# Kernel optimization log

Hardware: AMD Instinct MI355X
Metric: run time of the kernel (lower is better)

The kernel has to match this reference:

```python
import jax, jax.numpy as jnp
import numpy as np
import math

HIDDEN = 768
HEADS = 12
HEAD_DIM = HIDDEN // HEADS
BLOCK = 256
TOPK = 3
BATCH = 2
SEQ = 2048


def setup_inputs() -> dict:
    key = jax.random.key(0)
    ks = jax.random.split(key, 5)
    s = 1.0 / math.sqrt(HIDDEN)
    return {
        "hidden_states": jax.random.normal(ks[0], (BATCH, SEQ, HIDDEN), jnp.float32),
        "Wq": jax.random.normal(ks[1], (HIDDEN, HIDDEN), jnp.float32) * s,
        "Wk": jax.random.normal(ks[2], (HIDDEN, HIDDEN), jnp.float32) * s,
        "Wv": jax.random.normal(ks[3], (HIDDEN, HIDDEN), jnp.float32) * s,
        "Wo": jax.random.normal(ks[4], (HIDDEN, HIDDEN), jnp.float32) * s,
    }


def _rope(x, sin, cos):
    # x: [B, H, S, D]; rotate-half RoPE
    d2 = x.shape[-1] // 2
    x1, x2 = x[..., :d2], x[..., d2:]
    return x * cos + jnp.concatenate([-x2, x1], axis=-1) * sin


def reference(hidden_states, Wq, Wk, Wv, Wo):
    B, S, Hd = hidden_states.shape
    H, D, bs, K = HEADS, HEAD_DIM, BLOCK, TOPK
    nb = S // bs  # number of key blocks
    scale = 1.0 / math.sqrt(D)

    def split_heads(x):
        return x.reshape(B, S, H, D).transpose(0, 2, 1, 3)  # [B,H,S,D]

    q = split_heads(hidden_states @ Wq.T)
    k = split_heads(hidden_states @ Wk.T)
    v = split_heads(hidden_states @ Wv.T)

    # rotary embedding (standard rotate-half RoPE, base 10000)
    inv_freq = 1.0 / (10000.0 ** (jnp.arange(0, D, 2, dtype=jnp.float32) / D))
    ang = jnp.arange(S, dtype=jnp.float32)[:, None] * inv_freq[None, :]  # [S, D/2]
    emb = jnp.concatenate([ang, ang], axis=-1)  # [S, D]
    sin, cos = jnp.sin(emb), jnp.cos(emb)
    q = _rope(q, sin, cos)
    k = _rope(k, sin, cos)

    # mean-pooled block representations of keys: [B,H,nb,D]
    block_reps = k.reshape(B, H, nb, bs, D).mean(axis=3)

    # routing scores: per-token score against each block rep
    bscores = jnp.einsum('bhsd,bhnd->bhsn', q, block_reps) * scale  # [B,H,S,nb]
    pos = jnp.arange(S)
    cur = pos // bs                       # current block of each query, [S]
    blk = jnp.arange(nb)
    future = blk[None, None, None, :] > cur[None, None, :, None]
    bscores = jnp.where(future, -jnp.inf, bscores)
    # current block is force-selected (score set to dtype max)
    is_cur = blk[None, None, None, :] == cur[None, None, :, None]
    bscores = jnp.where(is_cur, jnp.finfo(bscores.dtype).max, bscores)

    _, topk_idx = jax.lax.top_k(bscores, min(K, nb))  # [B,H,S,K]
    selected = jnp.sum(jax.nn.one_hot(topk_idx, nb, dtype=jnp.float32), axis=-2) > 0  # [B,H,S,nb]

    # per-key-position mask: key t allowed iff its block is selected for query i,
    # and within the current block only t <= i (matches original truncation).
    sel_t = selected[:, :, :, cur]                          # [B,H,Sq,Sk]
    intra_ok = (cur[None, :] != cur[:, None]) | (pos[None, :] <= pos[:, None])  # [Sq,Sk]
    mask = sel_t & intra_ok[None, None]

    scores = jnp.einsum('bhqd,bhkd->bhqk', q, k) * scale
    scores = jnp.where(mask, scores, -jnp.inf)
    probs = jax.nn.softmax(scores, axis=-1)
    out = jnp.einsum('bhqk,bhkd->bhqd', probs, v)

    out = out.transpose(0, 2, 1, 3).reshape(B, S, Hd)
    return out @ Wo.T
```

## Files before the change

### kernel.cpp

```cpp
#include <hip/hip_runtime.h>
#include <math.h>


#define HID   768
#define NH    12
#define DH    64
#define SEQN  2048
#define BATCH 2
#define NTOK  (BATCH*SEQN)
#define NB    8
#define BLKSZ 256
#define NEG_INF (-__builtin_huge_valf())
#define POS_INF (__builtin_huge_valf())
#define LO_SCALE 2048.0f
#define LO_INV   (1.0f/2048.0f)
#define EXP2C    0.18033688f

#define SPLIT_ROWS 1024
#define NBH   (BATCH*NH)

typedef unsigned short u16;
typedef _Float16 v8hf __attribute__((ext_vector_type(8)));
typedef float    v4f  __attribute__((ext_vector_type(4)));

__device__ __forceinline__ u16 f2h(float x) {
    _Float16 h = (_Float16)x;
    return __builtin_bit_cast(u16, h);
}
__device__ __forceinline__ float h2f(u16 u) {
    return (float)__builtin_bit_cast(_Float16, u);
}
__device__ __forceinline__ v8hf ldhf8(const u16* p) {
    return *reinterpret_cast<const v8hf*>(p);
}
__device__ __forceinline__ void g2lds16(const u16* g, u16* l) {
    __builtin_amdgcn_global_load_lds(
        (const __attribute__((address_space(1))) void*)g,
        (__attribute__((address_space(3))) void*)l, 16, 0, 0);
}
#define MFMA16(a, b, c) __builtin_amdgcn_mfma_f32_16x16x32_f16(a, b, c, 0, 0, 0)

__device__ const int g_uord[48] = {
    46,47,44,45,15,
    42,43,40,41,14,
    38,39,36,37,13,
    34,35,32,33,12,
    30,31,28,29,11,
    26,27,24,25,10,
    22,23,20,21, 9,
    18,19,16,17, 8,
     7, 6, 5, 4, 3, 2, 1, 0
};

__global__ __launch_bounds__(256)
void preproc_k(const float* __restrict__ X,  const float* __restrict__ Wq,
               const float* __restrict__ Wk, const float* __restrict__ Wv,
               const float* __restrict__ Wo, float2* __restrict__ tab,
               u16* __restrict__ Xh, u16* __restrict__ Xl,
               u16* __restrict__ Wq2, u16* __restrict__ Wk2,
               u16* __restrict__ Wv2, u16* __restrict__ Wo2)
{
    const int NW = HID * HID;
    const int id = blockIdx.x;
    const int tid = threadIdx.x;
    if (id < 3072) {
        const int i = (id * 256 + tid) * 4;
        const float4 x4 = *(const float4*)&X[i];
        const float xf[4] = {x4.x, x4.y, x4.z, x4.w};
        ushort4 h4, l4;
        u16* hp = (u16*)&h4; u16* lp = (u16*)&l4;
        #pragma unroll
        for (int j = 0; j < 4; j++) {
            const u16 h = f2h(xf[j]);
            hp[j] = h;
            lp[j] = f2h((xf[j] - h2f(h)) * LO_SCALE);
        }
        *(ushort4*)&Xh[i] = h4;
        *(ushort4*)&Xl[i] = l4;
    } else if (id < 5376) {
        const int j4 = ((id - 3072) * 256 + tid) * 4;
        const int z = j4 / NW, i = j4 - z * NW;
        const float* src = (z == 0) ? Wq : (z == 1) ? Wk : (z == 2) ? Wv : Wo;
        u16* dst = (z == 0) ? Wq2 : (z == 1) ? Wk2 : (z == 2) ? Wv2 : Wo2;
        const float4 x4 = *(const float4*)&src[i];
        const float xf[4] = {x4.x, x4.y, x4.z, x4.w};
        ushort4 h4, l4;
        u16* hp = (u16*)&h4; u16* lp = (u16*)&l4;
        #pragma unroll
        for (int j = 0; j < 4; j++) {
            const u16 h = f2h(xf[j]);
            hp[j] = h;
            lp[j] = f2h((xf[j] - h2f(h)) * LO_SCALE);
        }
        *(ushort4*)&dst[i] = h4;
        *(ushort4*)&dst[i + NW] = l4;
    } else {
        const int i = (id - 5376) * 256 + tid;
        const int s = i >> 5, f = i & 31;
        const double y  = exp((double)f * (log(10000.0) / 32.0));
        const float yf = (float)y;
        const float invf = 1.0f / yf;
        const float ang  = (float)s * invf;
        tab[i] = make_float2((float)sin((double)ang), (float)cos((double)ang));
    }
}

__device__ __forceinline__
void qkv_mainloop(const u16* __restrict__ Ah, const u16* __restrict__ Al,
                  const u16* __restrict__ Bh, const u16* __restrict__ Bl,
                  int m0, int nb0, bool hasC0,
                  u16* As, u16* Bs, v4f acc01[2][4], v4f acc2[2][4])
{
    const int tid = threadIdx.x;
    const int w = tid >> 6, lane = tid & 63;
    const int col = lane & 15, quad = lane >> 4;
    const int AOFF = 128 * 64, BOFF = 64 * 64;

    int a_row[4], a_gl[4];
    #pragma unroll
    for (int r = 0; r < 4; r++) {
        const int g = r * 256 + tid;
        a_row[r] = g >> 3;
        a_gl[r]  = (g & 7) ^ (a_row[r] & 7);
    }
    int b_row[2], b_gl[2];
    #pragma unroll
    for (int r = 0; r < 2; r++) {
        const int g = r * 256 + tid;
        b_row[r] = g >> 3;
        b_gl[r]  = (g & 7) ^ (b_row[r] & 7);
    }

    for (int itc = 0; itc < HID / 64; itc++) {
        const int k0 = itc * 64;
        __syncthreads();
        #pragma unroll
        for (int r = 0; r < 4; r++)
            g2lds16(Ah + (size_t)(m0 + a_row[r]) * HID + k0 + a_gl[r] * 8,
                    &As[(r * 256 + w * 64) * 8]);
        if (hasC0) {
            #pragma unroll
            for (int r = 0; r < 4; r++)
                g2lds16(Al + (size_t)(m0 + a_row[r]) * HID + k0 + a_gl[r] * 8,
                        &As[AOFF + (r * 256 + w * 64) * 8]);
        }
        #pragma unroll
        for (int r = 0; r < 2; r++) {
            g2lds16(Bh + (size_t)(nb0 + b_row[r]) * HID + k0 + b_gl[r] * 8,
                    &Bs[(r * 256 + w * 64) * 8]);
            g2lds16(Bl + (size_t)(nb0 + b_row[r]) * HID + k0 + b_gl[r] * 8,
                    &Bs[BOFF + (r * 256 + w * 64) * 8]);
        }
        __syncthreads();
        #pragma unroll
        for (int ks = 0; ks < 2; ks++) {
            v8hf afh[2], afl[2], bfh[4], bfl[4];
            #pragma unroll
            for (int mt = 0; mt < 2; mt++) {
                const int row = w * 32 + mt * 16 + col;
                const int gph = (ks * 4 + quad) ^ (row & 7);
                afh[mt] = ldhf8(&As[row * 64 + gph * 8]);
                if (hasC0) afl[mt] = ldhf8(&As[AOFF + row * 64 + gph * 8]);
            }
            #pragma unroll
            for (int nt = 0; nt < 4; nt++) {
                const int row = nt * 16 + col;
                const int gph = (ks * 4 + quad) ^ (row & 7);
                bfh[nt] = ldhf8(&Bs[row * 64 + gph * 8]);
                bfl[nt] = ldhf8(&Bs[BOFF + row * 64 + gph * 8]);
            }
            #pragma unroll
            for (int mt = 0; mt < 2; mt++)
                #pragma unroll
                for (int nt = 0; nt < 4; nt++) {
                    if (hasC0)
                        acc01[mt][nt] = MFMA16(afl[mt], bfh[nt], acc01[mt][nt]);
                    acc01[mt][nt] = MFMA16(afh[mt], bfl[nt], acc01[mt][nt]);
                    acc2[mt][nt]  = MFMA16(afh[mt], bfh[nt], acc2[mt][nt]);
                }
        }
    }
    __syncthreads();
}

__global__ __launch_bounds__(256, 3)
void qkv_fused_gemm_k(const u16* __restrict__ Xh, const u16* __restrict__ Xl,
                      const u16* __restrict__ Wq2, const u16* __restrict__ Wk2,
                      const u16* __restrict__ Wv2, const float2* __restrict__ tab,
                      float* __restrict__ q32, u16* __restrict__ kh16,
                      u16* __restrict__ vth, float* __restrict__ partial)
{
    __shared__ u16 As[2 * 128 * 64];
    __shared__ u16 Bs[2 * 64 * 64];
    float (*psum)[64] = (float(*)[64])As;

    const int NW = HID * HID;
    const int id    = blockIdx.x;
    const int xcd   = id & 7, loc = id >> 3;
    const int mtile = xcd * 4 + (loc & 3);
    const int ntile = loc >> 2;
    const int m0  = mtile * 128;
    const int mat = ntile / 12;
    const int nb0 = (ntile - mat * 12) * 64;
    const u16* Bh = (mat == 0) ? Wq2 : (mat == 1) ? Wk2 : Wv2;

    v4f acc01[2][4] = {}, acc2[2][4] = {};
    qkv_mainloop(Xh, Xl, Bh, Bh + NW, m0, nb0, mat != 2, As, Bs, acc01, acc2);

    v4f acc[2][4];
    #pragma unroll
    for (int mt = 0; mt < 2; mt++)
        #pragma unroll
        for (int nt = 0; nt < 4; nt++)
            #pragma unroll
            for (int r = 0; r < 4; r++)
                acc[mt][nt][r] = acc01[mt][nt][r] * LO_INV + acc2[mt][nt][r];

    const int tid = threadIdx.x;
    const int w = tid >> 6, lane = tid & 63;
    const int col = lane & 15, quad = lane >> 4;
    const int b = m0 >> 11;
    const int h = nb0 >> 6;
    const size_t bh = (size_t)b * NH + h;

    if (mat == 2) {
        #pragma unroll
        for (int nt = 0; nt < 4; nt++) {
            const int d = nt * 16 + col;
            #pragma unroll
            for (int mt = 0; mt < 2; mt++) {
                const int m = m0 + w * 32 + mt * 16 + quad * 4;
                const int s = m & (SEQN - 1);
                ushort4 pk = make_ushort4(f2h(acc[mt][nt][0]), f2h(acc[mt][nt][1]),
                                          f2h(acc[mt][nt][2]), f2h(acc[mt][nt][3]));
                *(ushort4*)&vth[(bh * DH + d) * SEQN + s] = pk;
            }
        }
        return;
    }

    float vsum[4] = {0.f, 0.f, 0.f, 0.f};
    #pragma unroll
    for (int mt = 0; mt < 2; mt++) {
        #pragma unroll
        for (int nt = 0; nt < 4; nt++) {
            const int d = nt * 16 + col;
            #pragma unroll
            for (int r = 0; r < 4; r++) {
                const int m = m0 + w * 32 + mt * 16 + quad * 4 + r;
                const int s = m & (SEQN - 1);
                const float part = acc[mt][nt ^ 2][r];
                const float2 sc = tab[(s << 5) + (d & 31)];
                const float val = (d < 32) ? acc[mt][nt][r] * sc.y - part * sc.x
                                           : acc[mt][nt][r] * sc.y + part * sc.x;
                const size_t idx = (bh * SEQN + s) * DH + d;
                if (mat == 0) {
                    q32[idx] = val;
                } else {
                    kh16[idx] = f2h(val);
                    vsum[nt] += val;
                }
            }
        }
    }
    if (mat == 1) {
        #pragma unroll
        for (int nt = 0; nt < 4; nt++) {
            float v = vsum[nt];
            v += __shfl_xor(v, 16);
            v += __shfl_xor(v, 32);
            if (quad == 0) psum[w][nt * 16 + col] = v;
        }
        __syncthreads();
        if (tid < 64) {
            const float s4 = (psum[0][tid] + psum[1][tid])
                           + (psum[2][tid] + psum[3][tid]);
            const int nblk = (m0 & (SEQN - 1)) >> 8;
            const int half = (m0 >> 7) & 1;
            partial[((bh * NB + nblk) * 2 + half) * 64 + tid] = s4;
        }
    }
}

__global__ __launch_bounds__(256, 3)
void out_gemm_mfma_k(const u16* __restrict__ Ah, const u16* __restrict__ Wo2,
                     float* __restrict__ C)
{
    __shared__ u16 As[64 * 64];
    __shared__ u16 Bs[2 * 64 * 64];
    const int BOFF = 64 * 64;

    const int NW = HID * HID;
    const int id    = blockIdx.x;
    const int xcd   = id & 7, loc = id >> 3;
    const int mtile = xcd * 8 + (loc & 7);
    const int ntile = loc >> 3;
    const int m0 = mtile * 64, n0 = ntile * 64;
    const int tid = threadIdx.x;
    const int w = tid >> 6, lane = tid & 63;
    const int col = lane & 15, quad = lane >> 4;

    const int r0 = tid >> 3,         gl0 = (tid & 7) ^ (r0 & 7);
    const int r1 = (256 + tid) >> 3, gl1 = ((256 + tid) & 7) ^ (r1 & 7);

    const u16* Bhp = Wo2;
    const u16* Blp = Wo2 + NW;

    v4f accL[4] = {}, accH[4] = {};
    for (int itc = 0; itc < HID / 64; itc++) {
        const int k0 = itc * 64;
        __syncthreads();
        g2lds16(Ah  + (size_t)(m0 + r0) * HID + k0 + gl0 * 8, &As[(w * 64) * 8]);
        g2lds16(Ah  + (size_t)(m0 + r1) * HID + k0 + gl1 * 8, &As[(256 + w * 64) * 8]);
        g2lds16(Bhp + (size_t)(n0 + r0) * HID + k0 + gl0 * 8, &Bs[(w * 64) * 8]);
        g2lds16(Bhp + (size_t)(n0 + r1) * HID + k0 + gl1 * 8, &Bs[(256 + w * 64) * 8]);
        g2lds16(Blp + (size_t)(n0 + r0) * HID + k0 + gl0 * 8, &Bs[BOFF + (w * 64) * 8]);
        g2lds16(Blp + (size_t)(n0 + r1) * HID + k0 + gl1 * 8, &Bs[BOFF + (256 + w * 64) * 8]);
        __syncthreads();
        #pragma unroll
        for (int ks = 0; ks < 2; ks++) {
            const int arow = w * 16 + col;
            v8hf a = ldhf8(&As[arow * 64 + (((ks * 4 + quad) ^ (arow & 7))) * 8]);
            #pragma unroll
            for (int nt = 0; nt < 4; nt++) {
                const int row = nt * 16 + col;
                const int g = (ks * 4 + quad) ^ (row & 7);
                accH[nt] = MFMA16(a, ldhf8(&Bs[row * 64 + g * 8]), accH[nt]);
                accL[nt] = MFMA16(a, ldhf8(&Bs[BOFF + row * 64 + g * 8]), accL[nt]);
            }
        }
    }

    #pragma unroll
    for (int nt = 0; nt < 4; nt++)
        #pragma unroll
        for (int r = 0; r < 4; r++) {
            const int m = m0 + w * 16 + quad * 4 + r;
            C[(size_t)m * HID + n0 + nt * 16 + col] =
                accL[nt][r] * LO_INV + accH[nt][r];
        }
}

__global__ __launch_bounds__(256, 4)
void moba_attn_k(const float* __restrict__ q32, const u16* __restrict__ kh16,
                 const u16* __restrict__ vth, const float* __restrict__ partial,
                 u16* __restrict__ aoh, float* __restrict__ po,
                 float* __restrict__ ml)
{
    __shared__ u16 kbuf[2][64 * 64];
    __shared__ u16 vbuf[2][64 * 64];
    __shared__ u16 plds[4][16][64];
    unsigned* s_uni = (unsigned*)&vbuf[1][0];
    float (*rs)[DH] = (float(*)[DH])&kbuf[0][0];
    unsigned* msk   = (unsigned*)&kbuf[0][1024];

    const int id  = blockIdx.x;
    const int xcd = id & 7, loc = id >> 3;
    const int bh  = xcd * 3 + loc / 48;
    const int u   = g_uord[loc % 48];
    int qb, split, stride;
    if (u < 16) { qb = u;                 split = 0;          stride = 1; }
    else        { qb = 16 + ((u - 16) >> 1); split = (u - 16) & 1; stride = 2; }
    const int q0  = qb * 64;
    const int cur = q0 >> 8;
    const int tid = threadIdx.x;
    const int wave = tid >> 6, lane = tid & 63;
    const int col = lane & 15, quad = lane >> 4;
    const int qw0 = q0 + wave * 16;
    const int qpos = qw0 + col;
    const size_t bhS = (size_t)bh * SEQN;
    const size_t bhV = (size_t)bh * DH;

    if (tid == 0) *s_uni = 0;
    for (int idx = tid; idx < NB * DH; idx += 256) {
        const int n = idx >> 6, d = idx & 63;
        const float* pp = &partial[(size_t)((bh * NB + n) * 2) * 64 + d];
        const double s = (double)pp[0] + (double)pp[64];
        rs[n][d] = (float)(s * (1.0 / 256.0));
    }
    __syncthreads();

    if (tid < 64) {
        const float* qv = &q32[(bhS + q0 + tid) * DH];
        double sc[NB];
        #pragma unroll
        for (int n = 0; n < NB; n++) sc[n] = 0.0;
        for (int c = 0; c < 16; c++) {
            const float4 t = *(const float4*)&qv[c * 4];
            #pragma unroll
            for (int n = 0; n < NB; n++) {
                sc[n] += (double)t.x * (double)rs[n][c * 4 + 0];
                sc[n] += (double)t.y * (double)rs[n][c * 4 + 1];
                sc[n] += (double)t.z * (double)rs[n][c * 4 + 2];
                sc[n] += (double)t.w * (double)rs[n][c * 4 + 3];
            }
        }
        #pragma unroll
        for (int n = 0; n < NB; n++) sc[n] *= 0.125;
        for (int n = cur + 1; n < NB; n++) sc[n] = -1e300;
        sc[cur] = 1e300;
        unsigned m = 0;
        for (int p = 0; p < 3; p++) {
            int bi = -1; double bv = 0.0;
            for (int n = 0; n < NB; n++) {
                if ((m >> n) & 1) continue;
                if (bi < 0 || sc[n] > bv) { bi = n; bv = sc[n]; }
            }
            m |= 1u << bi;
        }
        msk[tid] = m;
    }
    __syncthreads();

    const unsigned mymask = msk[wave * 16 + col];
    unsigned uw = mymask;
    #pragma unroll
    for (int off = 1; off < 16; off <<= 1) uw |= __shfl_xor(uw, off);
    if (lane == 0) atomicOr(s_uni, uw);
    const unsigned wmask = __builtin_amdgcn_readfirstlane(uw);

    v8hf qh[2], ql[2];
    #pragma unroll
    for (int ks = 0; ks < 2; ks++) {
        const float* qp = &q32[(bhS + qw0 + col) * DH + ks * 32 + quad * 8];
        float4 f0 = *(const float4*)qp;
        float4 f1 = *(const float4*)(qp + 4);
        float qf[8] = {f0.x, f0.y, f0.z, f0.w, f1.x, f1.y, f1.z, f1.w};
        union { u16 u[8]; v8hf h; } uh, ul;
        #pragma unroll
        for (int j = 0; j < 8; j++) {
            u16 hb = f2h(qf[j]);
            uh.u[j] = hb;
            ul.u[j] = f2h((qf[j] - h2f(hb)) * LO_SCALE);
        }
        qh[ks] = uh.h; ql[ks] = ul.h;
    }
    __syncthreads();
    const unsigned uni = __builtin_amdgcn_readfirstlane(*s_uni);

    int n_nxt = __builtin_ctz(uni), c_nxt = 0;
    bool has_nxt = true;
    auto c2max = [&](int n) { return (n == cur) ? ((q0 + 63 - n * BLKSZ) >> 6) : 3; };
    auto advance1 = [&]() {
        if (c_nxt < c2max(n_nxt)) { c_nxt++; return; }
        for (int nn = n_nxt + 1; nn < NB; nn++)
            if ((uni >> nn) & 1) { n_nxt = nn; c_nxt = 0; return; }
        has_nxt = false;
    };
    for (int i = 0; i < split; i++) if (has_nxt) advance1();
    int n_cur = n_nxt, c_cur = c_nxt;
    const bool cur_valid = has_nxt;

    const size_t srow0 = (size_t)bh * SPLIT_ROWS + (q0 - SPLIT_ROWS);

    if (!cur_valid) {
        if (stride == 2) {
            if (quad == 0) {
                const size_t r = srow0 + wave * 16 + col;
                ml[(r * 2 + split) * 2 + 0] = NEG_INF;
                ml[(r * 2 + split) * 2 + 1] = 0.f;
            }
            #pragma unroll
            for (int nt = 0; nt < 4; nt++)
                #pragma unroll
                for (int r = 0; r < 4; r++) {
                    const size_t rq = srow0 + wave * 16 + quad * 4 + r;
                    po[(rq * 2 + split) * 64 + nt * 16 + col] = 0.f;
                }
        }
        return;
    }
    for (int i = 0; i < stride; i++) if (has_nxt) advance1();

    const int sg_row0 = tid >> 3;
    const int sg_gl0  = (tid & 7) ^ (sg_row0 & 7);
    const int sg_row1 = (256 + tid) >> 3;
    const int sg_gl1  = ((256 + tid) & 7) ^ (sg_row1 & 7);
    auto stage = [&](int n, int c2, int buf) {
        const int kb = n * BLKSZ + c2 * 64;
        u16* kd = (u16*)kbuf[buf];
        u16* vd = (u16*)vbuf[buf];
        const size_t ks0 = (bhS + kb + sg_row0) * DH + sg_gl0 * 8;
        const size_t ks1 = (bhS + kb + sg_row1) * DH + sg_gl1 * 8;
        const size_t vs0 = (bhV + sg_row0) * SEQN + kb + sg_gl0 * 8;
        const size_t vs1 = (bhV + sg_row1) * SEQN + kb + sg_gl1 * 8;
        g2lds16(kh16 + ks0, kd + (wave * 64) * 8);
        g2lds16(kh16 + ks1, kd + (256 + wave * 64) * 8);
        g2lds16(vth + vs0, vd + (wave * 64) * 8);
        g2lds16(vth + vs1, vd + (256 + wave * 64) * 8);
    };

    const v4f zero4 = {0.f, 0.f, 0.f, 0.f};
    v4f oacc[4] = {zero4, zero4, zero4, zero4};
    float m_i = NEG_INF, l_i = 0.f;
    const int psw = (col & 7) << 1;

    stage(n_cur, c_cur, 0);
    int t = 0;
    while (true) {
        __syncthreads();
        if (has_nxt) stage(n_nxt, c_nxt, (t + 1) & 1);

        const int n  = n_cur;
        const int kb = n * BLKSZ + c_cur * 64;
        const bool iscur = (n == cur);
        const float selinf = ((mymask >> n) & 1) ? 0.f : POS_INF;
        const bool need_mask = iscur && (kb + 63 > qw0);
        const u16* kd = (const u16*)kbuf[t & 1];
        const u16* vd = (const u16*)vbuf[t & 1];

        if ((wmask >> n) & 1) {
            v4f sf[4];
            __builtin_amdgcn_s_setprio(1);
            #pragma unroll
            for (int mt = 0; mt < 4; mt++) {
                const int row = mt * 16 + col;
                const int r7 = row & 7;
                v8hf kh0 = ldhf8(&kd[(row * 8 + (quad ^ r7)) * 8]);
                v8hf kh1 = ldhf8(&kd[(row * 8 + ((4 + quad) ^ r7)) * 8]);
                v4f c = zero4;
                c = MFMA16(kh0, ql[0], c);
                c = MFMA16(kh1, ql[1], c);
                #pragma unroll
                for (int r = 0; r < 4; r++) c[r] *= LO_INV;
                c = MFMA16(kh0, qh[0], c);
                c = MFMA16(kh1, qh[1], c);
                sf[mt] = c;
            }
            __builtin_amdgcn_s_setprio(0);

            if (need_mask) {
                #pragma unroll
                for (int mt = 0; mt < 4; mt++)
                    #pragma unroll
                    for (int r = 0; r < 4; r++) {
                        const int kidx = kb + mt * 16 + quad * 4 + r;
                        sf[mt][r] = (kidx <= qpos) ? sf[mt][r] : NEG_INF;
                    }
            }

            const float t0 = fmaxf(fmaxf(sf[0][0], sf[0][1]), fmaxf(sf[0][2], sf[0][3]));
            const float t1 = fmaxf(fmaxf(sf[1][0], sf[1][1]), fmaxf(sf[1][2], sf[1][3]));
            const float t2 = fmaxf(fmaxf(sf[2][0], sf[2][1]), fmaxf(sf[2][2], sf[2][3]));
            const float t3 = fmaxf(fmaxf(sf[3][0], sf[3][1]), fmaxf(sf[3][2], sf[3][3]));
            float rm = fmaxf(fmaxf(t0, t1), fmaxf(t2, t3));
            rm = fmaxf(rm, __shfl_xor(rm, 16));
            rm = fmaxf(rm, __shfl_xor(rm, 32));
            rm = rm - selinf;

            const bool fast = __all(rm <= m_i + 8.0f) != 0;
            float mnew = m_i, alpha = 1.f;
            if (!fast) {
                mnew  = fmaxf(m_i, rm);
                alpha = (m_i == NEG_INF) ? 0.f : exp2f((m_i - mnew) * EXP2C);
            }
            const float biasC = ((mnew == NEG_INF) ? 0.f : mnew * EXP2C) + selinf;

            float lmt[4];
            #pragma unroll
            for (int mt = 0; mt < 4; mt++) {
                ushort4 hv;
                float p0 = exp2f(fmaf(sf[mt][0], EXP2C, -biasC));
                float p1 = exp2f(fmaf(sf[mt][1], EXP2C, -biasC));
                float p2 = exp2f(fmaf(sf[mt][2], EXP2C, -biasC));
                float p3 = exp2f(fmaf(sf[mt][3], EXP2C, -biasC));
                hv.x = f2h(p0); hv.y = f2h(p1); hv.z = f2h(p2); hv.w = f2h(p3);
                lmt[mt] = (p0 + p1) + (p2 + p3);
                *(ushort4*)&plds[wave][col][((mt * 4 + quad) ^ psw) * 4] = hv;
            }
            float lsum = (lmt[0] + lmt[1]) + (lmt[2] + lmt[3]);
            lsum += __shfl_xor(lsum, 16);
            lsum += __shfl_xor(lsum, 32);

            if (fast) {
                l_i = l_i + lsum;
            } else {
                l_i = l_i * alpha + lsum;
                m_i = mnew;
                float ar[4];
                #pragma unroll
                for (int r = 0; r < 4; r++) ar[r] = __shfl(alpha, quad * 4 + r, 16);
                #pragma unroll
                for (int nt = 0; nt < 4; nt++)
                    #pragma unroll
                    for (int r = 0; r < 4; r++) oacc[nt][r] *= ar[r];
            }

            __threadfence_block();

            __builtin_amdgcn_s_setprio(1);
            #pragma unroll
            for (int ks2 = 0; ks2 < 2; ks2++) {
                v8hf ph = ldhf8(&plds[wave][col][((ks2 * 8 + quad * 2) ^ psw) * 4]);
                #pragma unroll
                for (int nt = 0; nt < 4; nt++) {
                    const int row = nt * 16 + col;
                    const int g = (ks2 * 4 + quad) ^ (row & 7);
                    v8hf vh = ldhf8(&vd[(row * 8 + g) * 8]);
                    oacc[nt] = MFMA16(ph, vh, oacc[nt]);
                }
            }
            __builtin_amdgcn_s_setprio(0);
        }

        if (!has_nxt) break;
        n_cur = n_nxt; c_cur = c_nxt;
        for (int i = 0; i < stride; i++) if (has_nxt) advance1();
        t++;
    }

    if (stride == 2) {
        if (quad == 0) {
            const size_t r = srow0 + wave * 16 + col;
            ml[(r * 2 + split) * 2 + 0] = m_i;
            ml[(r * 2 + split) * 2 + 1] = l_i;
        }
        #pragma unroll
        for (int nt = 0; nt < 4; nt++)
            #pragma unroll
            for (int r = 0; r < 4; r++) {
                const size_t rq = srow0 + wave * 16 + quad * 4 + r;
                po[(rq * 2 + split) * 64 + nt * 16 + col] = oacc[nt][r];
            }
        return;
    }

    const int b = bh / NH, h = bh % NH;
    const float invl = 1.f / l_i;
    float ir[4];
    #pragma unroll
    for (int r = 0; r < 4; r++) ir[r] = __shfl(invl, quad * 4 + r, 16);
    #pragma unroll
    for (int nt = 0; nt < 4; nt++)
        #pragma unroll
        for (int r = 0; r < 4; r++) {
            const int qi = qw0 + quad * 4 + r;
            const size_t idx = ((size_t)b * SEQN + qi) * HID + h * DH + nt * 16 + col;
            aoh[idx] = f2h(oacc[nt][r] * ir[r]);
        }
}

__global__ __launch_bounds__(256)
void attn_combine_k(const float* __restrict__ po, const float* __restrict__ ml,
                    u16* __restrict__ aoh)
{
    const int g = blockIdx.x * 256 + threadIdx.x;
    const int d = g & 63;
    const size_t row = (size_t)(g >> 6);
    const int bh = (int)(row >> 10);
    const int qlocal = (int)(row & 1023);
    const float m0 = ml[(row * 2 + 0) * 2 + 0], l0 = ml[(row * 2 + 0) * 2 + 1];
    const float m1 = ml[(row * 2 + 1) * 2 + 0], l1 = ml[(row * 2 + 1) * 2 + 1];
    const float m  = fmaxf(m0, m1);
    const float a0 = (m0 == NEG_INF) ? 0.f : exp2f((m0 - m) * EXP2C);
    const float a1 = (m1 == NEG_INF) ? 0.f : exp2f((m1 - m) * EXP2C);
    const float o  = po[(row * 2 + 0) * 64 + d] * a0
                   + po[(row * 2 + 1) * 64 + d] * a1;
    const float inv = 1.f / (l0 * a0 + l1 * a1);
    const int b = bh / NH, h = bh % NH;
    const int q = SPLIT_ROWS + qlocal;
    aoh[((size_t)b * SEQN + q) * HID + h * DH + d] = f2h(o * inv);
}

extern "C" void kernel_launch(void* const* d_in, const int* in_sizes, int n_in,
                              void* d_out, int out_size, void* d_ws, size_t ws_size,
                              hipStream_t stream)
{
    const float* X  = (const float*)d_in[0];
    const float* Wq = (const float*)d_in[1];
    const float* Wk = (const float*)d_in[2];
    const float* Wv = (const float*)d_in[3];
    const float* Wo = (const float*)d_in[4];
    float* out = (float*)d_out;

    char* p = (char*)d_ws;
    float* q32 = (float*)p;                p += (size_t)NTOK*HID*4;
    u16* kh16 = (u16*)p;                   p += (size_t)NTOK*HID*2;
    u16* vth  = (u16*)p;                   p += (size_t)NTOK*HID*2;
    u16* Xh   = (u16*)p;                   p += (size_t)NTOK*HID*2;
    u16* Xl   = (u16*)p;                   p += (size_t)NTOK*HID*2;
    u16* Wq2  = (u16*)p;                   p += (size_t)HID*HID*2*2;
    u16* Wk2  = (u16*)p;                   p += (size_t)HID*HID*2*2;
    u16* Wv2  = (u16*)p;                   p += (size_t)HID*HID*2*2;
    u16* Wo2  = (u16*)p;                   p += (size_t)HID*HID*2*2;
    float* partial = (float*)p;            p += (size_t)BATCH*NH*NB*2*64*4;
    float* reps    = (float*)p;            p += (size_t)BATCH*NH*NB*DH*4;
    unsigned* selm = (unsigned*)p;         p += (size_t)BATCH*NH*SEQN*4;
    float2* tab    = (float2*)p;           p += (size_t)SEQN*32*8;
    u16* aoh = Xh;
    (void)reps; (void)selm;

    float* po = (float*)Xl;
    float* ml = po + (size_t)NBH * SPLIT_ROWS * 2 * 64;

    preproc_k<<<dim3(5632), 256, 0, stream>>>(X, Wq, Wk, Wv, Wo, tab,
                                              Xh, Xl, Wq2, Wk2, Wv2, Wo2);

    qkv_fused_gemm_k<<<dim3(1152), 256, 0, stream>>>(
        Xh, Xl, Wq2, Wk2, Wv2, tab, q32, kh16, vth, partial);

    moba_attn_k<<<dim3(1152), 256, 0, stream>>>(
        q32, kh16, vth, partial, aoh, po, ml);

    attn_combine_k<<<dim3(6144), 256, 0, stream>>>(po, ml, aoh);

    out_gemm_mfma_k<<<dim3(768), 256, 0, stream>>>(aoh, Wo2, out);
}
```

Measured before the change: 201.0 us.

## Fuse split-K combine into attention via atomic flags; parallelize routing scores

Removes the separate attn_combine kernel. The second of each pair of split blocks to finish, decided by an atomic counter that is zeroed in preproc, merges the two partial outputs and writes the fp16 attention output directly. Separately, the q tile is staged once in LDS and the block-routing dot products are spread across all 256 threads instead of 64, with results kept in shared doubles. This saves a kernel launch and the extra pass over po/ml, at the cost of threadfence and atomic handshakes plus tail work in the last-finishing block.

```diff
diff --git a/kernel.cpp b/kernel.cpp
--- a/kernel.cpp
+++ b/kernel.cpp
@@ -58,7 +58,8 @@
                const float* __restrict__ Wo, float2* __restrict__ tab,
                u16* __restrict__ Xh, u16* __restrict__ Xl,
                u16* __restrict__ Wq2, u16* __restrict__ Wk2,
-               u16* __restrict__ Wv2, u16* __restrict__ Wo2)
+               u16* __restrict__ Wv2, u16* __restrict__ Wo2,
+               unsigned* __restrict__ flags)
 {
     const int NW = HID * HID;
     const int id = blockIdx.x;
@@ -95,6 +96,9 @@
         *(ushort4*)&dst[i] = h4;
         *(ushort4*)&dst[i + NW] = l4;
     } else {
+        if (id == 5376) {
+            for (int f = tid; f < NBH * 16; f += 256) flags[f] = 0;
+        }
         const int i = (id - 5376) * 256 + tid;
         const int s = i >> 5, f = i & 31;
         const double y  = exp((double)f * (log(10000.0) / 32.0));
@@ -345,14 +349,16 @@
 void moba_attn_k(const float* __restrict__ q32, const u16* __restrict__ kh16,
                  const u16* __restrict__ vth, const float* __restrict__ partial,
                  u16* __restrict__ aoh, float* __restrict__ po,
-                 float* __restrict__ ml)
+                 float* __restrict__ ml, unsigned* __restrict__ flags)
 {
     __shared__ u16 kbuf[2][64 * 64];
     __shared__ u16 vbuf[2][64 * 64];
     __shared__ u16 plds[4][16][64];
-    unsigned* s_uni = (unsigned*)&vbuf[1][0];
+    unsigned* s_uni = (unsigned*)&plds[0][0][0];
     float (*rs)[DH] = (float(*)[DH])&kbuf[0][0];
     unsigned* msk   = (unsigned*)&kbuf[0][1024];
+    double* dsc     = (double*)&kbuf[1][0];
+    float* qlds     = (float*)&vbuf[0][0];
 
     const int id  = blockIdx.x;
     const int xcd = id & 7, loc = id >> 3;
@@ -372,6 +378,12 @@
     const size_t bhV = (size_t)bh * DH;
 
     if (tid == 0) *s_uni = 0;
+    {
+        const float4* src = (const float4*)&q32[(bhS + q0) * DH];
+        float4* dst = (float4*)qlds;
+        #pragma unroll
+        for (int i = 0; i < 4; i++) dst[tid + i * 256] = src[tid + i * 256];
+    }
     for (int idx = tid; idx < NB * DH; idx += 256) {
         const int n = idx >> 6, d = idx & 63;
         const float* pp = &partial[(size_t)((bh * NB + n) * 2) * 64 + d];
@@ -380,23 +392,28 @@
     }
     __syncthreads();
 
+    #pragma unroll
+    for (int hh = 0; hh < 2; hh++) {
+        const int e = tid + hh * 256;
+        const int qi = e >> 3, n = e & 7;
+        const float4* qr4 = (const float4*)&qlds[qi * DH];
+        const float4* rr4 = (const float4*)&rs[n][0];
+        double s = 0.0;
+        for (int c = 0; c < 16; c++) {
+            const float4 a = qr4[c], b = rr4[c];
+            s += (double)a.x * (double)b.x;
+            s += (double)a.y * (double)b.y;
+            s += (double)a.z * (double)b.z;
+            s += (double)a.w * (double)b.w;
+        }
+        dsc[qi * 8 + n] = s;
+    }
+    __syncthreads();
+
     if (tid < 64) {
-        const float* qv = &q32[(bhS + q0 + tid) * DH];
         double sc[NB];
         #pragma unroll
-        for (int n = 0; n < NB; n++) sc[n] = 0.0;
-        for (int c = 0; c < 16; c++) {
-            const float4 t = *(const float4*)&qv[c * 4];
-            #pragma unroll
-            for (int n = 0; n < NB; n++) {
-                sc[n] += (double)t.x * (double)rs[n][c * 4 + 0];
-                sc[n] += (double)t.y * (double)rs[n][c * 4 + 1];
-                sc[n] += (double)t.z * (double)rs[n][c * 4 + 2];
-                sc[n] += (double)t.w * (double)rs[n][c * 4 + 3];
-            }
-        }
-        #pragma unroll
-        for (int n = 0; n < NB; n++) sc[n] *= 0.125;
+        for (int n = 0; n < NB; n++) sc[n] = dsc[tid * 8 + n] * 0.125;
         for (int n = cur + 1; n < NB; n++) sc[n] = -1e300;
         sc[cur] = 1e300;
         unsigned m = 0;
@@ -422,7 +439,7 @@
     v8hf qh[2], ql[2];
     #pragma unroll
     for (int ks = 0; ks < 2; ks++) {
-        const float* qp = &q32[(bhS + qw0 + col) * DH + ks * 32 + quad * 8];
+        const float* qp = &qlds[(wave * 16 + col) * DH + ks * 32 + quad * 8];
         float4 f0 = *(const float4*)qp;
         float4 f1 = *(const float4*)(qp + 4);
         float qf[8] = {f0.x, f0.y, f0.z, f0.w, f1.x, f1.y, f1.z, f1.w};
@@ -437,6 +454,40 @@
     }
     __syncthreads();
     const unsigned uni = __builtin_amdgcn_readfirstlane(*s_uni);
+
+    auto pair_combine = [&]() {
+        __threadfence();
+        unsigned* s_old = s_uni;
+        if (tid == 0) *s_old = atomicAdd(&flags[(bh << 4) + (qb - 16)], 1);
+        __syncthreads();
+        if (*s_old == 1) {
+            __threadfence();
+            const int row = tid >> 2;
+            const int d0  = (tid & 3) * 16;
+            const int q   = q0 + row;
+            const size_t srow = (size_t)bh * SPLIT_ROWS + (q - SPLIT_ROWS);
+            const float m0v = ml[(srow * 2 + 0) * 2 + 0];
+            const float l0v = ml[(srow * 2 + 0) * 2 + 1];
+            const float m1v = ml[(srow * 2 + 1) * 2 + 0];
+            const float l1v = ml[(srow * 2 + 1) * 2 + 1];
+            const float mm = fmaxf(m0v, m1v);
+            const float a0 = (m0v == NEG_INF) ? 0.f : exp2f((m0v - mm) * EXP2C);
+            const float a1 = (m1v == NEG_INF) ? 0.f : exp2f((m1v - mm) * EXP2C);
+            const float inv = 1.f / (l0v * a0 + l1v * a1);
+            const int b2 = bh / NH, h2 = bh % NH;
+            #pragma unroll
+            for (int j4 = 0; j4 < 4; j4++) {
+                const float4 p0 = *(const float4*)&po[(srow * 2 + 0) * 64 + d0 + j4 * 4];
+                const float4 p1 = *(const float4*)&po[(srow * 2 + 1) * 64 + d0 + j4 * 4];
+                ushort4 ov;
+                ov.x = f2h((p0.x * a0 + p1.x * a1) * inv);
+                ov.y = f2h((p0.y * a0 + p1.y * a1) * inv);
+                ov.z = f2h((p0.z * a0 + p1.z * a1) * inv);
+                ov.w = f2h((p0.w * a0 + p1.w * a1) * inv);
+                *(ushort4*)&aoh[((size_t)b2 * SEQN + q) * HID + h2 * DH + d0 + j4 * 4] = ov;
+            }
+        }
+    };
 
     int n_nxt = __builtin_ctz(uni), c_nxt = 0;
     bool has_nxt = true;
@@ -467,6 +518,7 @@
                     const size_t rq = srow0 + wave * 16 + quad * 4 + r;
                     po[(rq * 2 + split) * 64 + nt * 16 + col] = 0.f;
                 }
+            pair_combine();
         }
         return;
     }
@@ -622,6 +674,7 @@
                 const size_t rq = srow0 + wave * 16 + quad * 4 + r;
                 po[(rq * 2 + split) * 64 + nt * 16 + col] = oacc[nt][r];
             }
+        pair_combine();
         return;
     }
 
@@ -638,28 +691,6 @@
             const size_t idx = ((size_t)b * SEQN + qi) * HID + h * DH + nt * 16 + col;
             aoh[idx] = f2h(oacc[nt][r] * ir[r]);
         }
-}
-
-__global__ __launch_bounds__(256)
-void attn_combine_k(const float* __restrict__ po, const float* __restrict__ ml,
-                    u16* __restrict__ aoh)
-{
-    const int g = blockIdx.x * 256 + threadIdx.x;
-    const int d = g & 63;
-    const size_t row = (size_t)(g >> 6);
-    const int bh = (int)(row >> 10);
-    const int qlocal = (int)(row & 1023);
-    const float m0 = ml[(row * 2 + 0) * 2 + 0], l0 = ml[(row * 2 + 0) * 2 + 1];
-    const float m1 = ml[(row * 2 + 1) * 2 + 0], l1 = ml[(row * 2 + 1) * 2 + 1];
-    const float m  = fmaxf(m0, m1);
-    const float a0 = (m0 == NEG_INF) ? 0.f : exp2f((m0 - m) * EXP2C);
-    const float a1 = (m1 == NEG_INF) ? 0.f : exp2f((m1 - m) * EXP2C);
-    const float o  = po[(row * 2 + 0) * 64 + d] * a0
-                   + po[(row * 2 + 1) * 64 + d] * a1;
-    const float inv = 1.f / (l0 * a0 + l1 * a1);
-    const int b = bh / NH, h = bh % NH;
-    const int q = SPLIT_ROWS + qlocal;
-    aoh[((size_t)b * SEQN + q) * HID + h * DH + d] = f2h(o * inv);
 }
 
 extern "C" void kernel_launch(void* const* d_in, const int* in_sizes, int n_in,
@@ -685,24 +716,22 @@
     u16* Wo2  = (u16*)p;                   p += (size_t)HID*HID*2*2;
     float* partial = (float*)p;            p += (size_t)BATCH*NH*NB*2*64*4;
     float* reps    = (float*)p;            p += (size_t)BATCH*NH*NB*DH*4;
-    unsigned* selm = (unsigned*)p;         p += (size_t)BATCH*NH*SEQN*4;
+    unsigned* flags = (unsigned*)p;        p += (size_t)BATCH*NH*SEQN*4;
     float2* tab    = (float2*)p;           p += (size_t)SEQN*32*8;
     u16* aoh = Xh;
-    (void)reps; (void)selm;
+    (void)reps;
 
     float* po = (float*)Xl;
     float* ml = po + (size_t)NBH * SPLIT_ROWS * 2 * 64;
 
     preproc_k<<<dim3(5632), 256, 0, stream>>>(X, Wq, Wk, Wv, Wo, tab,
-                                              Xh, Xl, Wq2, Wk2, Wv2, Wo2);
+                                              Xh, Xl, Wq2, Wk2, Wv2, Wo2, flags);
 
     qkv_fused_gemm_k<<<dim3(1152), 256, 0, stream>>>(
         Xh, Xl, Wq2, Wk2, Wv2, tab, q32, kh16, vth, partial);
 
     moba_attn_k<<<dim3(1152), 256, 0, stream>>>(
-        q32, kh16, vth, partial, aoh, po, ml);
-
-    attn_combine_k<<<dim3(6144), 256, 0, stream>>>(po, ml, aoh);
+        q32, kh16, vth, partial, aoh, po, ml, flags);
 
     out_gemm_mfma_k<<<dim3(768), 256, 0, stream>>>(aoh, Wo2, out);
 }
```

New measurement: 345.6 us. 71.9% more time.
